# Optimization experiments

Measured on AMD Instinct MI355X. Metric: run time of the kernel, lower is better.

## Reference

```python
import jax, jax.numpy as jnp
import numpy as np

D_MODEL = 512
D_FF = 2048
D_K = 64
N_HEADS = 8
LN_EPS = 1e-5


def layer_norm(x, gamma, beta):
    mu = jnp.mean(x, axis=-1, keepdims=True)
    var = jnp.mean(jnp.square(x - mu), axis=-1, keepdims=True)
    return (x - mu) * jax.lax.rsqrt(var + LN_EPS) * gamma + beta


def setup_inputs() -> dict:
    key = jax.random.key(0)
    ks = jax.random.split(key, 8)
    B, S = 16, 1024
    s_in = 1.0 / np.sqrt(D_MODEL)
    s_ff = 1.0 / np.sqrt(D_FF)
    return {
        "x": jax.random.normal(ks[0], (B, S, D_MODEL), jnp.float32),
        # shared QKV projection (the module uses ONE linear for Q, K and V)
        "w_qkv": jax.random.uniform(ks[1], (D_MODEL, D_MODEL), jnp.float32, -s_in, s_in),
        "b_qkv": jnp.zeros((D_MODEL,), jnp.float32),
        "w_out": jax.random.uniform(ks[2], (D_MODEL, D_MODEL), jnp.float32, -s_in, s_in),
        "b_out": jnp.zeros((D_MODEL,), jnp.float32),
        "w1": jax.random.uniform(ks[3], (D_FF, D_MODEL), jnp.float32, -s_in, s_in),
        "b1": jnp.zeros((D_FF,), jnp.float32),
        "w2": jax.random.uniform(ks[4], (D_MODEL, D_FF), jnp.float32, -s_ff, s_ff),
        "b2": jnp.zeros((D_MODEL,), jnp.float32),
        "g1": jnp.ones((D_MODEL,), jnp.float32),
        "be1": jnp.zeros((D_MODEL,), jnp.float32),
        "g2": jnp.ones((D_MODEL,), jnp.float32),
        "be2": jnp.zeros((D_MODEL,), jnp.float32),
    }


def reference(x, w_qkv, b_qkv, w_out, b_out, w1, b1, w2, b2, g1, be1, g2, be2):
    B, S, _ = x.shape
    # --- MultiHeadAttention (shared linear for Q/K/V, dropout = identity) ---
    qkv = x @ w_qkv.T + b_qkv                       # [B,S,D]
    h = qkv.reshape(B, S, N_HEADS, D_K)             # Q = K = V
    scores = jnp.einsum("bqhd,bkhd->bhqk", h, h) / np.sqrt(D_K)
    probs = jax.nn.softmax(scores, axis=-1)
    ctx = jnp.einsum("bhqk,bkhd->bqhd", probs, h).reshape(B, S, D_MODEL)
    attn = ctx @ w_out.T + b_out
    # --- dual-LayerNorm residual #1: x = norm1(x) + norm1(attn) ---
    x = layer_norm(x, g1, be1) + layer_norm(attn, g1, be1)
    # --- FFN ---
    ffn = jax.nn.relu(x @ w1.T + b1) @ w2.T + b2
    # --- residual #2: x = x + norm2(ffn) ---
    return x + layer_norm(ffn, g2, be2)
```

## Files before the change

### kernel.cpp

```cpp
#include <hip/hip_runtime.h>
#include <hip/hip_bf16.h>
#include <stdint.h>


using bf16 = __bf16;
typedef __attribute__((ext_vector_type(2))) __bf16 bf16x2;
typedef __attribute__((ext_vector_type(4))) __bf16 bf16x4;
typedef __attribute__((ext_vector_type(8))) __bf16 bf16x8;
typedef __attribute__((ext_vector_type(4))) float floatx4;
typedef __attribute__((ext_vector_type(16))) float f32x16;

#define AS1 __attribute__((address_space(1)))
#define AS3 __attribute__((address_space(3)))

#define L2E 1.44269504088896340736f

constexpr int BN_ = 16, SQ_ = 1024, DM_ = 512, DFF_ = 2048, NH_ = 8, DK_ = 64;
constexpr int ROWS_ = BN_ * SQ_;

__global__ __launch_bounds__(256) void f2b_kernel(const float* __restrict__ in,
                                                  bf16* __restrict__ out, int n8) {
  int i = blockIdx.x * 256 + threadIdx.x;
  if (i >= n8) return;
  float4 a = ((const float4*)in)[2 * i];
  float4 b = ((const float4*)in)[2 * i + 1];
  bf16x8 o;
  o[0] = (bf16)a.x; o[1] = (bf16)a.y; o[2] = (bf16)a.z; o[3] = (bf16)a.w;
  o[4] = (bf16)b.x; o[5] = (bf16)b.y; o[6] = (bf16)b.z; o[7] = (bf16)b.w;
  ((bf16x8*)out)[i] = o;
}

template <int RELU>
__global__ __launch_bounds__(256) void gemm_bt(const bf16* __restrict__ A,
                                               const bf16* __restrict__ B,
                                               const float* __restrict__ bias,
                                               bf16* __restrict__ C,
                                               int M, int N, int K) {
  __shared__ bf16 As[128 * 32];
  __shared__ bf16 Bs[128 * 32];
  const int tid = threadIdx.x;
  const int lane = tid & 63;
  const int wv = tid >> 6;
  const int wr = wv >> 1, wc = wv & 1;
  const int r15 = lane & 15, g = lane >> 4;
  const int tileN = blockIdx.x * 128;
  const int tileM = blockIdx.y * 128;

  floatx4 acc[4][4] = {};

  const int nk = K >> 5;
  for (int kt = 0; kt < nk; ++kt) {
    const int k0 = kt << 5;
    __syncthreads();
#pragma unroll
    for (int is = 0; is < 2; ++is) {
      const int base = wv * 2048 + is * 1024;
      const int ob = base + lane * 16;
      const int row = ob >> 6;
      const int pslot = (ob >> 4) & 3;
      const int sslot = pslot ^ ((row >> 1) & 3);
      const bf16* ga = A + (size_t)(tileM + row) * K + (k0 + sslot * 8);
      __builtin_amdgcn_global_load_lds((AS1 uint32_t*)ga,
                                       (AS3 uint32_t*)((AS3 char*)As + base),
                                       16, 0, 0);
      const bf16* gb = B + (size_t)(tileN + row) * K + (k0 + sslot * 8);
      __builtin_amdgcn_global_load_lds((AS1 uint32_t*)gb,
                                       (AS3 uint32_t*)((AS3 char*)Bs + base),
                                       16, 0, 0);
    }
    __syncthreads();

    bf16x8 af[4], bfr[4];
#pragma unroll
    for (int m = 0; m < 4; ++m) {
      const int arow = wr * 64 + m * 16 + r15;
      const int ab = (arow * 64 + g * 16) ^ (((arow >> 1) & 3) << 4);
      af[m] = *(const bf16x8*)((const char*)As + ab);
    }
#pragma unroll
    for (int n = 0; n < 4; ++n) {
      const int brow = wc * 64 + n * 16 + r15;
      const int bb = (brow * 64 + g * 16) ^ (((brow >> 1) & 3) << 4);
      bfr[n] = *(const bf16x8*)((const char*)Bs + bb);
    }
#pragma unroll
    for (int m = 0; m < 4; ++m)
#pragma unroll
      for (int n = 0; n < 4; ++n)
        acc[m][n] = __builtin_amdgcn_mfma_f32_16x16x32_bf16(af[m], bfr[n],
                                                            acc[m][n], 0, 0, 0);
  }

#pragma unroll
  for (int n = 0; n < 4; ++n) {
    const int col = tileN + wc * 64 + n * 16 + r15;
    const float bv = bias[col];
#pragma unroll
    for (int m = 0; m < 4; ++m) {
      const int row0 = tileM + wr * 64 + m * 16 + g * 4;
#pragma unroll
      for (int j = 0; j < 4; ++j) {
        float v = acc[m][n][j] + bv;
        if (RELU) v = fmaxf(v, 0.f);
        C[(size_t)(row0 + j) * N + col] = (bf16)v;
      }
    }
  }
}

__global__ __launch_bounds__(256) void attn_kernel(const bf16* __restrict__ qkv,
                                                   bf16* __restrict__ ctx) {
  __shared__ char lds[16384];

  const int tid = threadIdx.x;
  const int lane = tid & 63;
  const int wv = tid >> 6;
  const int l31 = lane & 31;
  const int h = lane >> 5;
  const int b = blockIdx.z, hd = blockIdx.y, qt = blockIdx.x;
  const size_t headoff = (size_t)b * SQ_ * DM_ + hd * DK_;
  const int q0 = qt * 128 + wv * 32;

  const float QS = 0.125f * L2E;
  bf16x8 aq[4];
#pragma unroll
  for (int kd = 0; kd < 4; ++kd) {
    const bf16* gq = qkv + headoff + (size_t)(q0 + l31) * DM_ + kd * 16 + h * 8;
    bf16x8 v = *(const bf16x8*)gq;
#pragma unroll
    for (int e = 0; e < 8; ++e) v[e] = (bf16)((float)v[e] * QS);
    aq[kd] = v;
  }

  f32x16 o0 = {}, o1 = {};
  float mstate = -1e30f, lstate = 0.f;

  const uint32_t ldsb = (uint32_t)(uintptr_t)(AS3 char*)lds;

  uint32_t dstoff[2];
  const bf16* srcb[2];
#pragma unroll
  for (int is = 0; is < 2; ++is) {
    const int ob = is * 4096 + wv * 1024 + lane * 16;
    const int e0 = ob >> 1;
    const int srow = ((e0 >> 8) << 2) + ((e0 >> 4) & 3);
    const int dcol = ((e0 >> 6) & 3) * 16 + ((e0 >> 3) & 1) * 8;
    dstoff[is] = is * 4096 + wv * 1024;
    srcb[is] = qkv + headoff + (size_t)srow * DM_ + dcol;
  }

#define STAGE(buf, t)                                                          \
  {                                                                            \
    _Pragma("unroll")                                                          \
    for (int is = 0; is < 2; ++is) {                                           \
      __builtin_amdgcn_global_load_lds(                                        \
          (AS1 uint32_t*)(srcb[is] + (size_t)(t) * 64 * DM_),                  \
          (AS3 uint32_t*)((AS3 char*)lds + (buf) * 8192 + dstoff[is]), 16, 0, 0); \
    }                                                                          \
  }

  constexpr int NT = SQ_ / 64;
  STAGE(0, 0);

  for (int t = 0; t < NT; ++t) {
    const int cur = t & 1;
    __builtin_amdgcn_s_barrier();
    if (t + 1 < NT) {
      STAGE(cur ^ 1, t + 1);
      asm volatile("s_waitcnt vmcnt(2)" ::: "memory");
    } else {
      asm volatile("s_waitcnt vmcnt(0)" ::: "memory");
    }
    __builtin_amdgcn_s_barrier();
    __builtin_amdgcn_sched_barrier(0);

    const char* tile = (const char*)lds + cur * 8192;

    f32x16 s0v = {}, s1v = {};
    const char* pabase = tile + (l31 >> 2) * 512 + (l31 & 3) * 32 + h * 16;
    __builtin_amdgcn_s_setprio(1);
#pragma unroll
    for (int kd = 0; kd < 4; ++kd) {
      bf16x8 a0 = *(const bf16x8*)(pabase + kd * 128);
      bf16x8 a1 = *(const bf16x8*)(pabase + kd * 128 + 4096);
      s0v = __builtin_amdgcn_mfma_f32_32x32x16_bf16(a0, aq[kd], s0v, 0, 0, 0);
      s1v = __builtin_amdgcn_mfma_f32_32x32x16_bf16(a1, aq[kd], s1v, 0, 0, 0);
    }
    __builtin_amdgcn_s_setprio(0);

    float mx = s0v[0];
#pragma unroll
    for (int r = 1; r < 16; ++r) mx = fmaxf(mx, s0v[r]);
#pragma unroll
    for (int r = 0; r < 16; ++r) mx = fmaxf(mx, s1v[r]);
    mx = fmaxf(mx, __shfl_xor(mx, 32));
    if (!__all(mx - mstate <= 8.f)) {
      const float nm = fmaxf(mstate, mx);
      const float al = exp2f(mstate - nm);
      mstate = nm;
      lstate *= al;
#pragma unroll
      for (int r = 0; r < 16; ++r) { o0[r] *= al; o1[r] *= al; }
    }
    float rs = 0.f;
#pragma unroll
    for (int r = 0; r < 16; ++r) {
      float p = exp2f(s0v[r] - mstate);
      s0v[r] = p; rs += p;
    }
#pragma unroll
    for (int r = 0; r < 16; ++r) {
      float p = exp2f(s1v[r] - mstate);
      s1v[r] = p; rs += p;
    }
    rs += __shfl_xor(rs, 32);
    lstate += rs;

    uint32_t pf[4][4];
#pragma unroll
    for (int ks = 0; ks < 4; ++ks) {
      const int kb = (ks & 1) * 8;
      float v0, v1, v2, v3, v4, v5, v6, v7;
      if (ks < 2) {
        v0 = s0v[kb+0]; v1 = s0v[kb+1]; v2 = s0v[kb+2]; v3 = s0v[kb+3];
        v4 = s0v[kb+4]; v5 = s0v[kb+5]; v6 = s0v[kb+6]; v7 = s0v[kb+7];
      } else {
        v0 = s1v[kb+0]; v1 = s1v[kb+1]; v2 = s1v[kb+2]; v3 = s1v[kb+3];
        v4 = s1v[kb+4]; v5 = s1v[kb+5]; v6 = s1v[kb+6]; v7 = s1v[kb+7];
      }
      union { bf16x2 v; uint32_t u; } P0, P1, P2, P3;
      P0.v = bf16x2{(bf16)v0, (bf16)v1};
      P1.v = bf16x2{(bf16)v2, (bf16)v3};
      P2.v = bf16x2{(bf16)v4, (bf16)v5};
      P3.v = bf16x2{(bf16)v6, (bf16)v7};
      asm volatile("v_permlane32_swap_b32 %0, %1" : "+v"(P0.u), "+v"(P2.u));
      asm volatile("v_permlane32_swap_b32 %0, %1" : "+v"(P1.u), "+v"(P3.u));
      pf[ks][0] = P0.u;
      pf[ks][1] = P1.u;
      pf[ks][2] = P2.u;
      pf[ks][3] = P3.u;
    }

#pragma unroll
    for (int df = 0; df < 2; ++df) {
      const uint32_t vb = ldsb + cur * 8192 + df * 256 + (lane & 15) * 8 +
                          ((lane >> 4) & 1) * 128 + (lane >> 5) * 1024;
      bf16x4 lo[4], hi[4];
#pragma unroll
      for (int ks = 0; ks < 4; ++ks) {
        asm volatile("ds_read_b64_tr_b16 %0, %2\n\t"
                     "ds_read_b64_tr_b16 %1, %2 offset:512"
                     : "=&v"(lo[ks]), "=&v"(hi[ks])
                     : "v"(vb + ks * 2048));
      }
      asm volatile("s_waitcnt lgkmcnt(0)" ::: "memory");
      __builtin_amdgcn_sched_barrier(0);
      __builtin_amdgcn_s_setprio(1);
#pragma unroll
      for (int ks = 0; ks < 4; ++ks) {
        union { struct { bf16x4 l, h; } p; bf16x8 v; } av;
        av.p.l = lo[ks]; av.p.h = hi[ks];
        union { uint32_t u[4]; bf16x8 v; } bv;
        bv.u[0] = pf[ks][0]; bv.u[1] = pf[ks][1];
        bv.u[2] = pf[ks][2]; bv.u[3] = pf[ks][3];
        if (df == 0)
          o0 = __builtin_amdgcn_mfma_f32_32x32x16_bf16(av.v, bv.v, o0, 0, 0, 0);
        else
          o1 = __builtin_amdgcn_mfma_f32_32x32x16_bf16(av.v, bv.v, o1, 0, 0, 0);
      }
      __builtin_amdgcn_s_setprio(0);
    }
  }
#undef STAGE

  __syncthreads();
  const float invl = 1.f / lstate;
  char* wb = (char*)lds + wv * 4096;
#pragma unroll
  for (int df = 0; df < 2; ++df)
#pragma unroll
    for (int t = 0; t < 4; ++t) {
      const f32x16& ov = df ? o1 : o0;
      bf16x4 pkt;
      pkt[0] = (bf16)(ov[4*t+0] * invl);
      pkt[1] = (bf16)(ov[4*t+1] * invl);
      pkt[2] = (bf16)(ov[4*t+2] * invl);
      pkt[3] = (bf16)(ov[4*t+3] * invl);
      const int byte = (l31 * 128 + df * 64 + t * 16 + h * 8) ^ ((l31 & 7) << 4);
      *(bf16x4*)(wb + byte) = pkt;
    }
#pragma unroll
  for (int ps = 0; ps < 4; ++ps) {
    const int qr = ps * 8 + (lane >> 3);
    const int byte = (qr * 128 + (lane & 7) * 16) ^ ((qr & 7) << 4);
    bf16x8 vv = *(const bf16x8*)(wb + byte);
    bf16* dst = ctx + (size_t)(b * SQ_ + q0 + qr) * DM_ + hd * 64 + (lane & 7) * 8;
    *(bf16x8*)dst = vv;
  }
}

__global__ __launch_bounds__(256) void dual_ln_kernel(const float* __restrict__ x,
                                                      const bf16* __restrict__ attn,
                                                      const float* __restrict__ g1,
                                                      const float* __restrict__ be1,
                                                      bf16* __restrict__ out) {
  const int row = blockIdx.x * 4 + (threadIdx.x >> 6);
  const int lane = threadIdx.x & 63;
  const float* xr = x + (size_t)row * DM_ + lane * 8;
  float xs[8], as_[8];
  float4 t0 = ((const float4*)xr)[0];
  float4 t1 = ((const float4*)xr)[1];
  xs[0] = t0.x; xs[1] = t0.y; xs[2] = t0.z; xs[3] = t0.w;
  xs[4] = t1.x; xs[5] = t1.y; xs[6] = t1.z; xs[7] = t1.w;
  bf16x8 av = *(const bf16x8*)(attn + (size_t)row * DM_ + lane * 8);
#pragma unroll
  for (int e = 0; e < 8; ++e) as_[e] = (float)av[e];
  float sx = 0, sx2 = 0, sa = 0, sa2 = 0;
#pragma unroll
  for (int e = 0; e < 8; ++e) {
    sx += xs[e]; sx2 += xs[e] * xs[e];
    sa += as_[e]; sa2 += as_[e] * as_[e];
  }
#pragma unroll
  for (int off = 1; off < 64; off <<= 1) {
    sx += __shfl_xor(sx, off);  sx2 += __shfl_xor(sx2, off);
    sa += __shfl_xor(sa, off);  sa2 += __shfl_xor(sa2, off);
  }
  const float inv = 1.f / (float)DM_;
  const float mux = sx * inv, mua = sa * inv;
  const float rx = rsqrtf(fmaxf(sx2 * inv - mux * mux, 0.f) + 1e-5f);
  const float ra = rsqrtf(fmaxf(sa2 * inv - mua * mua, 0.f) + 1e-5f);
  bf16x8 ov;
#pragma unroll
  for (int e = 0; e < 8; ++e) {
    const int c = lane * 8 + e;
    const float val = ((xs[e] - mux) * rx + (as_[e] - mua) * ra) * g1[c] + 2.f * be1[c];
    ov[e] = (bf16)val;
  }
  *(bf16x8*)(out + (size_t)row * DM_ + lane * 8) = ov;
}

__global__ __launch_bounds__(256) void final_ln_kernel(const bf16* __restrict__ x1,
                                                       const bf16* __restrict__ ffn,
                                                       const float* __restrict__ g2,
                                                       const float* __restrict__ be2,
                                                       float* __restrict__ out) {
  const int row = blockIdx.x * 4 + (threadIdx.x >> 6);
  const int lane = threadIdx.x & 63;
  bf16x8 xv = *(const bf16x8*)(x1 + (size_t)row * DM_ + lane * 8);
  bf16x8 fv = *(const bf16x8*)(ffn + (size_t)row * DM_ + lane * 8);
  float fs[8];
#pragma unroll
  for (int e = 0; e < 8; ++e) fs[e] = (float)fv[e];
  float sf = 0, sf2 = 0;
#pragma unroll
  for (int e = 0; e < 8; ++e) { sf += fs[e]; sf2 += fs[e] * fs[e]; }
#pragma unroll
  for (int off = 1; off < 64; off <<= 1) {
    sf += __shfl_xor(sf, off);  sf2 += __shfl_xor(sf2, off);
  }
  const float inv = 1.f / (float)DM_;
  const float mu = sf * inv;
  const float rs = rsqrtf(fmaxf(sf2 * inv - mu * mu, 0.f) + 1e-5f);
  float ov[8];
#pragma unroll
  for (int e = 0; e < 8; ++e) {
    const int c = lane * 8 + e;
    ov[e] = (float)xv[e] + (fs[e] - mu) * rs * g2[c] + be2[c];
  }
  float* orow = out + (size_t)row * DM_ + lane * 8;
  float4 o0 = {ov[0], ov[1], ov[2], ov[3]};
  float4 o1 = {ov[4], ov[5], ov[6], ov[7]};
  ((float4*)orow)[0] = o0;
  ((float4*)orow)[1] = o1;
}

extern "C" void kernel_launch(void* const* d_in, const int* in_sizes, int n_in,
                              void* d_out, int out_size, void* d_ws, size_t ws_size,
                              hipStream_t stream) {
  const float* x     = (const float*)d_in[0];
  const float* w_qkv = (const float*)d_in[1];
  const float* b_qkv = (const float*)d_in[2];
  const float* w_out = (const float*)d_in[3];
  const float* b_out = (const float*)d_in[4];
  const float* w1    = (const float*)d_in[5];
  const float* b1    = (const float*)d_in[6];
  const float* w2    = (const float*)d_in[7];
  const float* b2    = (const float*)d_in[8];
  const float* g1    = (const float*)d_in[9];
  const float* be1   = (const float*)d_in[10];
  const float* g2    = (const float*)d_in[11];
  const float* be2   = (const float*)d_in[12];
  float* out = (float*)d_out;

  char* ws = (char*)d_ws;
  const size_t o_wqkv = 0;
  const size_t o_wout = o_wqkv + (size_t)DM_ * DM_ * 2;
  const size_t o_w1   = o_wout + (size_t)DM_ * DM_ * 2;
  const size_t o_w2   = o_w1 + (size_t)DFF_ * DM_ * 2;
  const size_t o_A    = o_w2 + (size_t)DM_ * DFF_ * 2;
  const size_t o_B    = o_A + (size_t)ROWS_ * DM_ * 2;
  const size_t o_C    = o_B + (size_t)ROWS_ * DM_ * 2;
  const size_t o_D    = o_C + (size_t)ROWS_ * DM_ * 2;
  const size_t need   = o_D + (size_t)ROWS_ * DFF_ * 2;
  if (ws_size < need) return;

  bf16* wqkv_bf = (bf16*)(ws + o_wqkv);
  bf16* wout_bf = (bf16*)(ws + o_wout);
  bf16* w1_bf   = (bf16*)(ws + o_w1);
  bf16* w2_bf   = (bf16*)(ws + o_w2);
  bf16* bufA    = (bf16*)(ws + o_A);
  bf16* bufB    = (bf16*)(ws + o_B);
  bf16* bufC    = (bf16*)(ws + o_C);
  bf16* bufD    = (bf16*)(ws + o_D);

  f2b_kernel<<<dim3((ROWS_ * DM_ / 8 + 255) / 256), dim3(256), 0, stream>>>(x, bufA, ROWS_ * DM_ / 8);
  f2b_kernel<<<dim3((DM_ * DM_ / 8 + 255) / 256), dim3(256), 0, stream>>>(w_qkv, wqkv_bf, DM_ * DM_ / 8);
  f2b_kernel<<<dim3((DM_ * DM_ / 8 + 255) / 256), dim3(256), 0, stream>>>(w_out, wout_bf, DM_ * DM_ / 8);
  f2b_kernel<<<dim3((DFF_ * DM_ / 8 + 255) / 256), dim3(256), 0, stream>>>(w1, w1_bf, DFF_ * DM_ / 8);
  f2b_kernel<<<dim3((DM_ * DFF_ / 8 + 255) / 256), dim3(256), 0, stream>>>(w2, w2_bf, DM_ * DFF_ / 8);

  gemm_bt<0><<<dim3(DM_ / 128, ROWS_ / 128), dim3(256), 0, stream>>>(bufA, wqkv_bf, b_qkv, bufB, ROWS_, DM_, DM_);

  attn_kernel<<<dim3(SQ_ / 128, NH_, BN_), dim3(256), 0, stream>>>(bufB, bufA);

  gemm_bt<0><<<dim3(DM_ / 128, ROWS_ / 128), dim3(256), 0, stream>>>(bufA, wout_bf, b_out, bufC, ROWS_, DM_, DM_);

  dual_ln_kernel<<<dim3(ROWS_ / 4), dim3(256), 0, stream>>>(x, bufC, g1, be1, bufB);

  gemm_bt<1><<<dim3(DFF_ / 128, ROWS_ / 128), dim3(256), 0, stream>>>(bufB, w1_bf, b1, bufD, ROWS_, DFF_, DM_);

  gemm_bt<0><<<dim3(DM_ / 128, ROWS_ / 128), dim3(256), 0, stream>>>(bufD, w2_bf, b2, bufC, ROWS_, DM_, DFF_);

  final_ln_kernel<<<dim3(ROWS_ / 4), dim3(256), 0, stream>>>(bufB, bufC, g2, be2, out);
}
```

Measured before the change: 259.6 us.

## Double-buffer GEMM LDS tiles to overlap global loads with MFMA

Turns the bf16 GEMM main loop into a two-stage pipeline. The next K-tile is loaded into a second LDS buffer with global_load_lds while MFMAs run on the current one, and partial vmcnt waits plus raw s_barriers replace the two __syncthreads per iteration. It also hoists the source pointers and swizzled LDS offsets out of the loop. The goal is to hide global-load latency, at the cost of doubled LDS (32KB per block), which may lower occupancy.

```diff
diff --git a/kernel.cpp b/kernel.cpp
--- a/kernel.cpp
+++ b/kernel.cpp
@@ -36,8 +36,7 @@
                                                const float* __restrict__ bias,
                                                bf16* __restrict__ C,
                                                int M, int N, int K) {
-  __shared__ bf16 As[128 * 32];
-  __shared__ bf16 Bs[128 * 32];
+  __shared__ char glds[32768];
   const int tid = threadIdx.x;
   const int lane = tid & 63;
   const int wv = tid >> 6;
@@ -48,48 +47,78 @@
 
   floatx4 acc[4][4] = {};
 
+  uint32_t dstoff[2];
+  const bf16* srcA[2];
+  const bf16* srcB[2];
+#pragma unroll
+  for (int is = 0; is < 2; ++is) {
+    const int base = wv * 2048 + is * 1024;
+    const int ob = base + lane * 16;
+    const int row = ob >> 6;
+    const int pslot = (ob >> 4) & 3;
+    const int sslot = pslot ^ ((row >> 1) & 3);
+    dstoff[is] = base;
+    srcA[is] = A + (size_t)(tileM + row) * K + sslot * 8;
+    srcB[is] = B + (size_t)(tileN + row) * K + sslot * 8;
+  }
+
+#define GSTAGE(buf, kt)                                                         \
+  {                                                                             \
+    _Pragma("unroll")                                                           \
+    for (int is = 0; is < 2; ++is) {                                            \
+      __builtin_amdgcn_global_load_lds(                                         \
+          (AS1 uint32_t*)(srcA[is] + (kt) * 32),                                \
+          (AS3 uint32_t*)((AS3 char*)glds + (buf) * 8192 + dstoff[is]), 16, 0, 0); \
+      __builtin_amdgcn_global_load_lds(                                         \
+          (AS1 uint32_t*)(srcB[is] + (kt) * 32),                                \
+          (AS3 uint32_t*)((AS3 char*)glds + 16384 + (buf) * 8192 + dstoff[is]), \
+          16, 0, 0);                                                            \
+    }                                                                           \
+  }
+
+  uint32_t aoff[4], boff[4];
+#pragma unroll
+  for (int m = 0; m < 4; ++m) {
+    const int arow = wr * 64 + m * 16 + r15;
+    aoff[m] = (uint32_t)((arow * 64 + g * 16) ^ (((arow >> 1) & 3) << 4));
+  }
+#pragma unroll
+  for (int n = 0; n < 4; ++n) {
+    const int brow = wc * 64 + n * 16 + r15;
+    boff[n] = (uint32_t)((brow * 64 + g * 16) ^ (((brow >> 1) & 3) << 4));
+  }
+
   const int nk = K >> 5;
+  GSTAGE(0, 0);
+
   for (int kt = 0; kt < nk; ++kt) {
-    const int k0 = kt << 5;
-    __syncthreads();
-#pragma unroll
-    for (int is = 0; is < 2; ++is) {
-      const int base = wv * 2048 + is * 1024;
-      const int ob = base + lane * 16;
-      const int row = ob >> 6;
-      const int pslot = (ob >> 4) & 3;
-      const int sslot = pslot ^ ((row >> 1) & 3);
-      const bf16* ga = A + (size_t)(tileM + row) * K + (k0 + sslot * 8);
-      __builtin_amdgcn_global_load_lds((AS1 uint32_t*)ga,
-                                       (AS3 uint32_t*)((AS3 char*)As + base),
-                                       16, 0, 0);
-      const bf16* gb = B + (size_t)(tileN + row) * K + (k0 + sslot * 8);
-      __builtin_amdgcn_global_load_lds((AS1 uint32_t*)gb,
-                                       (AS3 uint32_t*)((AS3 char*)Bs + base),
-                                       16, 0, 0);
-    }
-    __syncthreads();
+    const int cur = kt & 1;
+    if (kt + 1 < nk) {
+      GSTAGE(cur ^ 1, kt + 1);
+      asm volatile("s_waitcnt vmcnt(4)" ::: "memory");
+    } else {
+      asm volatile("s_waitcnt vmcnt(0)" ::: "memory");
+    }
+    __builtin_amdgcn_s_barrier();
+    __builtin_amdgcn_sched_barrier(0);
+
+    const char* Ac = (const char*)glds + cur * 8192;
+    const char* Bc = (const char*)glds + 16384 + cur * 8192;
 
     bf16x8 af[4], bfr[4];
 #pragma unroll
-    for (int m = 0; m < 4; ++m) {
-      const int arow = wr * 64 + m * 16 + r15;
-      const int ab = (arow * 64 + g * 16) ^ (((arow >> 1) & 3) << 4);
-      af[m] = *(const bf16x8*)((const char*)As + ab);
-    }
-#pragma unroll
-    for (int n = 0; n < 4; ++n) {
-      const int brow = wc * 64 + n * 16 + r15;
-      const int bb = (brow * 64 + g * 16) ^ (((brow >> 1) & 3) << 4);
-      bfr[n] = *(const bf16x8*)((const char*)Bs + bb);
-    }
+    for (int m = 0; m < 4; ++m) af[m] = *(const bf16x8*)(Ac + aoff[m]);
+#pragma unroll
+    for (int n = 0; n < 4; ++n) bfr[n] = *(const bf16x8*)(Bc + boff[n]);
 #pragma unroll
     for (int m = 0; m < 4; ++m)
 #pragma unroll
       for (int n = 0; n < 4; ++n)
         acc[m][n] = __builtin_amdgcn_mfma_f32_16x16x32_bf16(af[m], bfr[n],
                                                             acc[m][n], 0, 0, 0);
-  }
+    __builtin_amdgcn_s_barrier();
+  }
+#undef GSTAGE
 
 #pragma unroll
   for (int n = 0; n < 4; ++n) {
```

After: 238.5 us. -8.2%, faster.
